# Optimization experiments

Hardware: AMD Instinct MI355X
Metric: run time of the kernel (lower is better)

## Reference

```python
import jax, jax.numpy as jnp
import numpy as np

# Model constants (from TinyRecursiveModel defaults)
IN = 200        # input feature dim (hard-coded Linear(200, d_model))
D = 64          # d_model
NH = 2          # nhead (head_dim = 32); with seq_len=1 attention is trivial
FF = 64         # dim_feedforward
LAYERS = 2      # TransformerEncoder num_layers
STEPS = 16      # recursion_steps
B = 65536       # batch size
EPS = 1e-5      # torch LayerNorm eps


def setup_inputs() -> dict:
    key = jax.random.key(0)
    ks = jax.random.split(key, 14)
    w = lambda k, shape, s=0.05: (jax.random.normal(k, shape, jnp.float32) * s)
    return {
        "x": jax.random.normal(ks[0], (B, IN), jnp.float32),
        # input_proj: Linear(200, 64)
        "input_w": w(ks[1], (D, IN)), "input_b": w(ks[2], (D,)),
        # per-layer MHA: packed in_proj (q,k,v) and out_proj, stacked over LAYERS
        "Wqkv": w(ks[3], (LAYERS, 3 * D, D)), "bqkv": w(ks[4], (LAYERS, 3 * D)),
        "Wo": w(ks[5], (LAYERS, D, D)), "bo": w(ks[6], (LAYERS, D)),
        "ln1_g": jnp.ones((LAYERS, D), jnp.float32), "ln1_b": jnp.zeros((LAYERS, D), jnp.float32),
        # per-layer FFN: Linear(64,64) -> relu -> Linear(64,64)
        "W1": w(ks[7], (LAYERS, FF, D)), "b1": w(ks[8], (LAYERS, FF)),
        "W2": w(ks[9], (LAYERS, D, FF)), "b2": w(ks[10], (LAYERS, D)),
        "ln2_g": jnp.ones((LAYERS, D), jnp.float32), "ln2_b": jnp.zeros((LAYERS, D), jnp.float32),
        # output_proj: Linear(64, 1)
        "out_w": w(ks[11], (1, D)), "out_b": w(ks[12], (1,)),
    }


def _ln(x, g, b):
    m = jnp.mean(x, axis=-1, keepdims=True)
    v = jnp.var(x, axis=-1, keepdims=True)
    return (x - m) * jax.lax.rsqrt(v + EPS) * g + b


def reference(x, input_w, input_b, Wqkv, bqkv, Wo, bo, ln1_g, ln1_b,
              W1, b1, W2, b2, ln2_g, ln2_b, out_w, out_b):
    h = x @ input_w.T + input_b  # [B, D]; seq dim of size 1 is kept implicit

    def layer(h, l):
        # seq_len == 1: softmax over a single key is identically 1, so the
        # attention output equals V exactly (Q/K have zero influence & zero grad).
        Wv = Wqkv[l, 2 * D:3 * D]
        bv = bqkv[l, 2 * D:3 * D]
        v = h @ Wv.T + bv                     # [B, D]
        sa = v @ Wo[l].T + bo[l]              # out_proj
        h = _ln(h + sa, ln1_g[l], ln1_b[l])   # post-norm (torch default)
        ff = jax.nn.relu(h @ W1[l].T + b1[l]) @ W2[l].T + b2[l]
        return _ln(h + ff, ln2_g[l], ln2_b[l])

    def step(h, _):
        for l in range(LAYERS):  # 2 structurally distinct layers
            h = layer(h, l)
        return h, None

    h, _ = jax.lax.scan(step, h, None, length=STEPS)
    out = h @ out_w.T + out_b  # [B, 1]
    return out[:, 0]           # squeeze -> [B]
```

## Files before the change

### kernel.cpp

```cpp
#include <hip/hip_runtime.h>


using f16x8 = __attribute__((ext_vector_type(8))) _Float16;
using f16x2 = __attribute__((ext_vector_type(2))) _Float16;
using f32x4 = __attribute__((ext_vector_type(4))) float;

#define DI __device__ __forceinline__

namespace {

constexpr int RS = 144;
constexpr float EPS = 1e-5f;

DI unsigned pkrtz(float a, float b) {
#if __has_builtin(__builtin_amdgcn_cvt_pkrtz)
  return __builtin_bit_cast(unsigned, __builtin_amdgcn_cvt_pkrtz(a, b));
#else
  unsigned r;
  asm("v_cvt_pkrtz_f16_f32 %0, %1, %2" : "=v"(r) : "v"(a), "v"(b));
  return r;
#endif
}

DI f16x8 cvt8h(f32x4 a, f32x4 b) {
  f16x8 r;
  r[0] = (_Float16)a[0]; r[1] = (_Float16)a[1];
  r[2] = (_Float16)a[2]; r[3] = (_Float16)a[3];
  r[4] = (_Float16)b[0]; r[5] = (_Float16)b[1];
  r[6] = (_Float16)b[2]; r[7] = (_Float16)b[3];
  return r;
}

DI unsigned pkmax0(unsigned t) {
  unsigned r;
  asm("v_pk_max_f16 %0, %1, 0" : "=v"(r) : "v"(t));
  return r;
}

DI void swap16(unsigned& a, unsigned& b) {
#if __has_builtin(__builtin_amdgcn_permlane16_swap)
  auto r = __builtin_amdgcn_permlane16_swap(a, b, false, false);
  a = r[0]; b = r[1];
#else
  unsigned ax = (unsigned)__shfl_xor((int)a, 16);
  unsigned bx = (unsigned)__shfl_xor((int)b, 16);
  bool odd = (threadIdx.x & 16) != 0;
  unsigned na = odd ? bx : a;
  unsigned nb = odd ? b : ax;
  a = na; b = nb;
#endif
}
DI void swap32(unsigned& a, unsigned& b) {
#if __has_builtin(__builtin_amdgcn_permlane32_swap)
  auto r = __builtin_amdgcn_permlane32_swap(a, b, false, false);
  a = r[0]; b = r[1];
#else
  unsigned ax = (unsigned)__shfl_xor((int)a, 32);
  unsigned bx = (unsigned)__shfl_xor((int)b, 32);
  bool hi = (threadIdx.x & 32) != 0;
  unsigned na = hi ? bx : a;
  unsigned nb = hi ? b : ax;
  a = na; b = nb;
#endif
}

DI float reduce4(float x) {
  unsigned a = __builtin_bit_cast(unsigned, x), b = a;
  swap16(a, b);
  float x1 = __builtin_bit_cast(float, a) + __builtin_bit_cast(float, b);
  unsigned c = __builtin_bit_cast(unsigned, x1), d = c;
  swap32(c, d);
  return __builtin_bit_cast(float, c) + __builtin_bit_cast(float, d);
}

union BU {
  unsigned u[8];
  struct { f16x8 b0, b1; } f;
};

template <bool RELU>
DI void packacc(const f32x4 (&acc)[4], BU& o) {
#pragma unroll
  for (int tp = 0; tp < 4; ++tp) {
    unsigned p0 = pkrtz(acc[tp][0], acc[tp][1]);
    unsigned p1 = pkrtz(acc[tp][2], acc[tp][3]);
    if (RELU) { p0 = pkmax0(p0); p1 = pkmax0(p1); }
    o.u[2 * tp + 0] = p0;
    o.u[2 * tp + 1] = p1;
  }
}

struct WFrag { f16x8 f[4][2]; };

DI WFrag loadW(const float* W, int l15, int g) {
  WFrag w;
#pragma unroll
  for (int tp = 0; tp < 4; ++tp)
#pragma unroll
    for (int s = 0; s < 2; ++s) {
      const float* p = W + (16 * tp + l15) * 64 + 32 * s + 4 * g;
      w.f[tp][s] = cvt8h(*(const f32x4*)p, *(const f32x4*)(p + 16));
    }
  return w;
}

DI f32x4 mfma(f16x8 a, f16x8 b, f32x4 c) {
  return __builtin_amdgcn_mfma_f32_16x16x32_f16(a, b, c, 0, 0, 0);
}

DI void lnorm2(const f32x4 (&aA)[4], const f32x4 (&aB)[4], const float* gb,
               int g, f32x4 (&hA)[4], f32x4 (&hB)[4]) {
  float sA = 0.f, qA = 0.f, sB = 0.f, qB = 0.f;
#pragma unroll
  for (int tp = 0; tp < 4; ++tp)
#pragma unroll
    for (int r = 0; r < 4; ++r) {
      float xa = aA[tp][r]; sA += xa; qA = fmaf(xa, xa, qA);
      float xb = aB[tp][r]; sB += xb; qB = fmaf(xb, xb, qB);
    }
  sA = reduce4(sA); qA = reduce4(qA);
  sB = reduce4(sB); qB = reduce4(qB);
  float mA = sA * 0.015625f, mB = sB * 0.015625f;
  float rA = rsqrtf(fmaf(qA, 0.015625f, -mA * mA) + EPS);
  float rB = rsqrtf(fmaf(qB, 0.015625f, -mB * mB) + EPS);
  float uA = -mA * rA, uB = -mB * rB;
  const f32x4* gv = (const f32x4*)gb;
#pragma unroll
  for (int tp = 0; tp < 4; ++tp) {
    f32x4 gg = gv[4 * tp + g];
    f32x4 bb = gv[16 + 4 * tp + g];
#pragma unroll
    for (int r = 0; r < 4; ++r) {
      hA[tp][r] = fmaf(fmaf(aA[tp][r], rA, uA), gg[r], bb[r]);
      hB[tp][r] = fmaf(fmaf(aB[tp][r], rB, uB), gg[r], bb[r]);
    }
  }
}

struct alignas(16) Smem {
  char mats[4][64 * RS];
};

DI void do_layer(f32x4 (&hA)[4], f32x4 (&hB)[4], BU& bA, BU& bB,
                 const WFrag& wvo, const char* w1b, const char* w2b,
                 const float* prm, int g) {
  asm("" : "+r"(prm));
  const f32x4* pv = (const f32x4*)prm;
  f32x4 aA[4], aB[4];
#pragma unroll
  for (int tp = 0; tp < 4; ++tp) {
    aA[tp] = mfma(wvo.f[tp][1], bA.f.b1, mfma(wvo.f[tp][0], bA.f.b0, hA[tp]));
    aB[tp] = mfma(wvo.f[tp][1], bB.f.b1, mfma(wvo.f[tp][0], bB.f.b0, hB[tp]));
    f32x4 bv = pv[4 * tp + g];
    aA[tp] += bv; aB[tp] += bv;
  }
  lnorm2(aA, aB, prm + 192, g, hA, hB);
  packacc<false>(hA, bA); packacc<false>(hB, bB);
#pragma unroll
  for (int tp = 0; tp < 4; ++tp) {
    f16x8 a0 = *(const f16x8*)(w1b + tp * 16 * RS);
    f16x8 a1 = *(const f16x8*)(w1b + tp * 16 * RS + 64);
    f32x4 cin = pv[16 + 4 * tp + g];
    aA[tp] = mfma(a1, bA.f.b1, mfma(a0, bA.f.b0, cin));
    aB[tp] = mfma(a1, bB.f.b1, mfma(a0, bB.f.b0, cin));
  }
  packacc<true>(aA, bA); packacc<true>(aB, bB);
#pragma unroll
  for (int tp = 0; tp < 4; ++tp) {
    f16x8 a0 = *(const f16x8*)(w2b + tp * 16 * RS);
    f16x8 a1 = *(const f16x8*)(w2b + tp * 16 * RS + 64);
    aA[tp] = mfma(a1, bA.f.b1, mfma(a0, bA.f.b0, hA[tp]));
    aB[tp] = mfma(a1, bB.f.b1, mfma(a0, bB.f.b0, hB[tp]));
    f32x4 bv = pv[32 + 4 * tp + g];
    aA[tp] += bv; aB[tp] += bv;
  }
  lnorm2(aA, aB, prm + 320, g, hA, hB);
  packacc<false>(hA, bA); packacc<false>(hB, bB);
}

__global__ __launch_bounds__(256) void precompute_kernel(
    const float* __restrict__ Wqkv, const float* __restrict__ bqkv,
    const float* __restrict__ Wo, const float* __restrict__ bo,
    const float* __restrict__ b1, const float* __restrict__ b2,
    const float* __restrict__ ln1_g, const float* __restrict__ ln1_b,
    const float* __restrict__ ln2_g, const float* __restrict__ ln2_b,
    float* __restrict__ ws) {
  __shared__ float wv[4096];
  __shared__ float wo[4096];
  const int l = blockIdx.x;
  const float* Wv  = Wqkv + l * (192 * 64) + 128 * 64;
  const float* WoL = Wo + l * 4096;
  for (int e = threadIdx.x; e < 4096; e += 256) { wv[e] = Wv[e]; wo[e] = WoL[e]; }
  __syncthreads();
  float* wvo = ws + l * 4096;
  const int i = threadIdx.x >> 2, j0 = (threadIdx.x & 3) * 16;
  float acc[16];
#pragma unroll
  for (int jj = 0; jj < 16; ++jj) acc[jj] = 0.f;
  for (int k = 0; k < 64; ++k) {
    float a = wo[i * 64 + k];
#pragma unroll
    for (int jj = 0; jj < 16; ++jj) acc[jj] = fmaf(a, wv[k * 64 + j0 + jj], acc[jj]);
  }
#pragma unroll
  for (int jj = 0; jj < 16; ++jj) wvo[i * 64 + j0 + jj] = acc[jj];
  float* prm = ws + 2 * 4096 + l * 448;
  if (threadIdx.x < 64) {
    const int i2 = threadIdx.x;
    const float* bv = bqkv + l * 192 + 128;
    float s = bo[l * 64 + i2];
    for (int k = 0; k < 64; ++k) s = fmaf(wo[i2 * 64 + k], bv[k], s);
    prm[i2]       = s;
    prm[64 + i2]  = b1[l * 64 + i2];
    prm[128 + i2] = b2[l * 64 + i2];
    prm[192 + i2] = ln1_g[l * 64 + i2];
    prm[256 + i2] = ln1_b[l * 64 + i2];
    prm[320 + i2] = ln2_g[l * 64 + i2];
    prm[384 + i2] = ln2_b[l * 64 + i2];
  }
}

__global__ __launch_bounds__(256, 2) void trm8_kernel(
    const float* __restrict__ x, const float* __restrict__ input_w,
    const float* __restrict__ input_b, const float* __restrict__ W1,
    const float* __restrict__ W2, const float* __restrict__ out_w,
    const float* __restrict__ out_b, const float* __restrict__ ws,
    float* __restrict__ out) {
  __shared__ Smem sm;
  const int tid = threadIdx.x;
  const int w = tid >> 6, lane = tid & 63;
  const int l15 = lane & 15, g = lane >> 4;
  const int row0 = blockIdx.x * 128 + w * 32;

  {
    const float* srcs[4] = {W1, W1 + 4096, W2, W2 + 4096};
#pragma unroll
    for (int m = 0; m < 4; ++m) {
      char* dst = sm.mats[m];
      const float* src = srcs[m];
      for (int e = tid; e < 512; e += 256) {
        int row = e >> 3, q = e & 7, s = q >> 2, gq = q & 3;
        const float* p = src + row * 64 + 32 * s + 4 * gq;
        *(f16x8*)(dst + row * RS + 64 * s + 16 * gq) =
            cvt8h(*(const f32x4*)p, *(const f32x4*)(p + 16));
      }
    }
  }

  WFrag wvo0 = loadW(ws, l15, g);
  WFrag wvo1 = loadW(ws + 4096, l15, g);

  const char* w1b0 = sm.mats[0] + l15 * RS + 16 * g;
  const char* w1b1 = sm.mats[1] + l15 * RS + 16 * g;
  const char* w2b0 = sm.mats[2] + l15 * RS + 16 * g;
  const char* w2b1 = sm.mats[3] + l15 * RS + 16 * g;
  const float* prm0 = ws + 2 * 4096;
  const float* prm1 = ws + 2 * 4096 + 448;

  f32x4 hA[4], hB[4];
#pragma unroll
  for (int tp = 0; tp < 4; ++tp) {
    f32x4 ib = *(const f32x4*)(input_b + 16 * tp + 4 * g);
    hA[tp] = ib; hB[tp] = ib;
  }
  {
    const float* xA = x + (size_t)(row0 + l15) * 200;
    const float* xB = xA + 16 * 200;
    const f32x4 zero = {0.f, 0.f, 0.f, 0.f};
    for (int s7 = 0; s7 < 7; ++s7) {
      int kb = 32 * s7 + 8 * g;
      bool v0 = kb < 200;
      f32x4 xa0 = v0 ? *(const f32x4*)(xA + kb) : zero;
      f32x4 xa1 = v0 ? *(const f32x4*)(xA + kb + 4) : zero;
      f32x4 xb0 = v0 ? *(const f32x4*)(xB + kb) : zero;
      f32x4 xb1 = v0 ? *(const f32x4*)(xB + kb + 4) : zero;
      f16x8 bfA = cvt8h(xa0, xa1);
      f16x8 bfB = cvt8h(xb0, xb1);
#pragma unroll
      for (int tp = 0; tp < 4; ++tp) {
        const float* wr = input_w + (16 * tp + l15) * 200;
        f32x4 wa = v0 ? *(const f32x4*)(wr + kb) : zero;
        f32x4 wb = v0 ? *(const f32x4*)(wr + kb + 4) : zero;
        f16x8 af = cvt8h(wa, wb);
        hA[tp] = mfma(af, bfA, hA[tp]);
        hB[tp] = mfma(af, bfB, hB[tp]);
      }
    }
  }
  BU bA, bB;
  packacc<false>(hA, bA); packacc<false>(hB, bB);
  __syncthreads();

#pragma unroll 1
  for (int step = 0; step < 16; ++step) {
    do_layer(hA, hB, bA, bB, wvo0, w1b0, w2b0, prm0, g);
    do_layer(hA, hB, bA, bB, wvo1, w1b1, w2b1, prm1, g);
  }

  float pA = 0.f, pB = 0.f;
#pragma unroll
  for (int tp = 0; tp < 4; ++tp) {
    f32x4 ow = *(const f32x4*)(out_w + 16 * tp + 4 * g);
#pragma unroll
    for (int r = 0; r < 4; ++r) {
      pA = fmaf(hA[tp][r], ow[r], pA);
      pB = fmaf(hB[tp][r], ow[r], pB);
    }
  }
  pA += __shfl_xor(pA, 16); pA += __shfl_xor(pA, 32);
  pB += __shfl_xor(pB, 16); pB += __shfl_xor(pB, 32);
  if (lane < 16) {
    float ob = out_b[0];
    out[row0 + l15]      = pA + ob;
    out[row0 + 16 + l15] = pB + ob;
  }
}

}

extern "C" void kernel_launch(void* const* d_in, const int* in_sizes, int n_in,
                              void* d_out, int out_size, void* d_ws, size_t ws_size,
                              hipStream_t stream) {
  const float* x       = (const float*)d_in[0];
  const float* input_w = (const float*)d_in[1];
  const float* input_b = (const float*)d_in[2];
  const float* Wqkv    = (const float*)d_in[3];
  const float* bqkv    = (const float*)d_in[4];
  const float* Wo      = (const float*)d_in[5];
  const float* bo      = (const float*)d_in[6];
  const float* ln1_g   = (const float*)d_in[7];
  const float* ln1_b   = (const float*)d_in[8];
  const float* W1      = (const float*)d_in[9];
  const float* b1      = (const float*)d_in[10];
  const float* W2      = (const float*)d_in[11];
  const float* b2      = (const float*)d_in[12];
  const float* ln2_g   = (const float*)d_in[13];
  const float* ln2_b   = (const float*)d_in[14];
  const float* out_w   = (const float*)d_in[15];
  const float* out_b   = (const float*)d_in[16];
  float* out = (float*)d_out;
  float* ws  = (float*)d_ws;

  hipLaunchKernelGGL(precompute_kernel, dim3(2), dim3(256), 0, stream,
                     Wqkv, bqkv, Wo, bo, b1, b2, ln1_g, ln1_b, ln2_g, ln2_b, ws);
  hipLaunchKernelGGL(trm8_kernel, dim3(512), dim3(256), 0, stream,
                     x, input_w, input_b, W1, W2, out_w, out_b, ws, out);
}
```

Measured before the change: 108.2 us.

## Process four 16-row tiles per wavefront with 128-thread blocks

```diff
diff --git a/kernel.cpp b/kernel.cpp
--- a/kernel.cpp
+++ b/kernel.cpp
@@ -2,7 +2,6 @@
 
 
 using f16x8 = __attribute__((ext_vector_type(8))) _Float16;
-using f16x2 = __attribute__((ext_vector_type(2))) _Float16;
 using f32x4 = __attribute__((ext_vector_type(4))) float;
 
 #define DI __device__ __forceinline__
@@ -108,22 +107,32 @@
   return __builtin_amdgcn_mfma_f32_16x16x32_f16(a, b, c, 0, 0, 0);
 }
 
-DI void lnorm2(const f32x4 (&aA)[4], const f32x4 (&aB)[4], const float* gb,
-               int g, f32x4 (&hA)[4], f32x4 (&hB)[4]) {
-  float sA = 0.f, qA = 0.f, sB = 0.f, qB = 0.f;
+DI void lnorm4(const f32x4 (&a0)[4], const f32x4 (&a1)[4],
+               const f32x4 (&a2)[4], const f32x4 (&a3)[4],
+               const float* gb, int g,
+               f32x4 (&h0)[4], f32x4 (&h1)[4], f32x4 (&h2)[4], f32x4 (&h3)[4]) {
+  float s0 = 0.f, q0 = 0.f, s1 = 0.f, q1 = 0.f;
+  float s2 = 0.f, q2 = 0.f, s3 = 0.f, q3 = 0.f;
 #pragma unroll
   for (int tp = 0; tp < 4; ++tp)
 #pragma unroll
     for (int r = 0; r < 4; ++r) {
-      float xa = aA[tp][r]; sA += xa; qA = fmaf(xa, xa, qA);
-      float xb = aB[tp][r]; sB += xb; qB = fmaf(xb, xb, qB);
-    }
-  sA = reduce4(sA); qA = reduce4(qA);
-  sB = reduce4(sB); qB = reduce4(qB);
-  float mA = sA * 0.015625f, mB = sB * 0.015625f;
-  float rA = rsqrtf(fmaf(qA, 0.015625f, -mA * mA) + EPS);
-  float rB = rsqrtf(fmaf(qB, 0.015625f, -mB * mB) + EPS);
-  float uA = -mA * rA, uB = -mB * rB;
+      float x0 = a0[tp][r]; s0 += x0; q0 = fmaf(x0, x0, q0);
+      float x1 = a1[tp][r]; s1 += x1; q1 = fmaf(x1, x1, q1);
+      float x2 = a2[tp][r]; s2 += x2; q2 = fmaf(x2, x2, q2);
+      float x3 = a3[tp][r]; s3 += x3; q3 = fmaf(x3, x3, q3);
+    }
+  s0 = reduce4(s0); q0 = reduce4(q0);
+  s1 = reduce4(s1); q1 = reduce4(q1);
+  s2 = reduce4(s2); q2 = reduce4(q2);
+  s3 = reduce4(s3); q3 = reduce4(q3);
+  float m0 = s0 * 0.015625f, m1 = s1 * 0.015625f;
+  float m2 = s2 * 0.015625f, m3 = s3 * 0.015625f;
+  float r0 = rsqrtf(fmaf(q0, 0.015625f, -m0 * m0) + EPS);
+  float r1 = rsqrtf(fmaf(q1, 0.015625f, -m1 * m1) + EPS);
+  float r2 = rsqrtf(fmaf(q2, 0.015625f, -m2 * m2) + EPS);
+  float r3 = rsqrtf(fmaf(q3, 0.015625f, -m3 * m3) + EPS);
+  float u0 = -m0 * r0, u1 = -m1 * r1, u2 = -m2 * r2, u3 = -m3 * r3;
   const f32x4* gv = (const f32x4*)gb;
 #pragma unroll
   for (int tp = 0; tp < 4; ++tp) {
@@ -131,8 +140,10 @@
     f32x4 bb = gv[16 + 4 * tp + g];
 #pragma unroll
     for (int r = 0; r < 4; ++r) {
-      hA[tp][r] = fmaf(fmaf(aA[tp][r], rA, uA), gg[r], bb[r]);
-      hB[tp][r] = fmaf(fmaf(aB[tp][r], rB, uB), gg[r], bb[r]);
+      h0[tp][r] = fmaf(fmaf(a0[tp][r], r0, u0), gg[r], bb[r]);
+      h1[tp][r] = fmaf(fmaf(a1[tp][r], r1, u1), gg[r], bb[r]);
+      h2[tp][r] = fmaf(fmaf(a2[tp][r], r2, u2), gg[r], bb[r]);
+      h3[tp][r] = fmaf(fmaf(a3[tp][r], r3, u3), gg[r], bb[r]);
     }
   }
 }
@@ -141,41 +152,48 @@
   char mats[4][64 * RS];
 };
 
-DI void do_layer(f32x4 (&hA)[4], f32x4 (&hB)[4], BU& bA, BU& bB,
-                 const WFrag& wvo, const char* w1b, const char* w2b,
-                 const float* prm, int g) {
+DI void do_layer(f32x4 (&h0)[4], f32x4 (&h1)[4], f32x4 (&h2)[4], f32x4 (&h3)[4],
+                 BU& b0, BU& b1, BU& b2, BU& b3, const WFrag& wvo,
+                 const char* w1b, const char* w2b, const float* prm, int g) {
   asm("" : "+r"(prm));
   const f32x4* pv = (const f32x4*)prm;
-  f32x4 aA[4], aB[4];
-#pragma unroll
-  for (int tp = 0; tp < 4; ++tp) {
-    aA[tp] = mfma(wvo.f[tp][1], bA.f.b1, mfma(wvo.f[tp][0], bA.f.b0, hA[tp]));
-    aB[tp] = mfma(wvo.f[tp][1], bB.f.b1, mfma(wvo.f[tp][0], bB.f.b0, hB[tp]));
+  f32x4 a0[4], a1[4], a2[4], a3[4];
+#pragma unroll
+  for (int tp = 0; tp < 4; ++tp) {
     f32x4 bv = pv[4 * tp + g];
-    aA[tp] += bv; aB[tp] += bv;
-  }
-  lnorm2(aA, aB, prm + 192, g, hA, hB);
-  packacc<false>(hA, bA); packacc<false>(hB, bB);
-#pragma unroll
-  for (int tp = 0; tp < 4; ++tp) {
-    f16x8 a0 = *(const f16x8*)(w1b + tp * 16 * RS);
-    f16x8 a1 = *(const f16x8*)(w1b + tp * 16 * RS + 64);
+    a0[tp] = mfma(wvo.f[tp][1], b0.f.b1, mfma(wvo.f[tp][0], b0.f.b0, h0[tp])) + bv;
+    a1[tp] = mfma(wvo.f[tp][1], b1.f.b1, mfma(wvo.f[tp][0], b1.f.b0, h1[tp])) + bv;
+    a2[tp] = mfma(wvo.f[tp][1], b2.f.b1, mfma(wvo.f[tp][0], b2.f.b0, h2[tp])) + bv;
+    a3[tp] = mfma(wvo.f[tp][1], b3.f.b1, mfma(wvo.f[tp][0], b3.f.b0, h3[tp])) + bv;
+  }
+  lnorm4(a0, a1, a2, a3, prm + 192, g, h0, h1, h2, h3);
+  packacc<false>(h0, b0); packacc<false>(h1, b1);
+  packacc<false>(h2, b2); packacc<false>(h3, b3);
+#pragma unroll
+  for (int tp = 0; tp < 4; ++tp) {
+    f16x8 wa0 = *(const f16x8*)(w1b + tp * 16 * RS);
+    f16x8 wa1 = *(const f16x8*)(w1b + tp * 16 * RS + 64);
     f32x4 cin = pv[16 + 4 * tp + g];
-    aA[tp] = mfma(a1, bA.f.b1, mfma(a0, bA.f.b0, cin));
-    aB[tp] = mfma(a1, bB.f.b1, mfma(a0, bB.f.b0, cin));
-  }
-  packacc<true>(aA, bA); packacc<true>(aB, bB);
-#pragma unroll
-  for (int tp = 0; tp < 4; ++tp) {
-    f16x8 a0 = *(const f16x8*)(w2b + tp * 16 * RS);
-    f16x8 a1 = *(const f16x8*)(w2b + tp * 16 * RS + 64);
-    aA[tp] = mfma(a1, bA.f.b1, mfma(a0, bA.f.b0, hA[tp]));
-    aB[tp] = mfma(a1, bB.f.b1, mfma(a0, bB.f.b0, hB[tp]));
+    a0[tp] = mfma(wa1, b0.f.b1, mfma(wa0, b0.f.b0, cin));
+    a1[tp] = mfma(wa1, b1.f.b1, mfma(wa0, b1.f.b0, cin));
+    a2[tp] = mfma(wa1, b2.f.b1, mfma(wa0, b2.f.b0, cin));
+    a3[tp] = mfma(wa1, b3.f.b1, mfma(wa0, b3.f.b0, cin));
+  }
+  packacc<true>(a0, b0); packacc<true>(a1, b1);
+  packacc<true>(a2, b2); packacc<true>(a3, b3);
+#pragma unroll
+  for (int tp = 0; tp < 4; ++tp) {
+    f16x8 wa0 = *(const f16x8*)(w2b + tp * 16 * RS);
+    f16x8 wa1 = *(const f16x8*)(w2b + tp * 16 * RS + 64);
     f32x4 bv = pv[32 + 4 * tp + g];
-    aA[tp] += bv; aB[tp] += bv;
-  }
-  lnorm2(aA, aB, prm + 320, g, hA, hB);
-  packacc<false>(hA, bA); packacc<false>(hB, bB);
+    a0[tp] = mfma(wa1, b0.f.b1, mfma(wa0, b0.f.b0, h0[tp])) + bv;
+    a1[tp] = mfma(wa1, b1.f.b1, mfma(wa0, b1.f.b0, h1[tp])) + bv;
+    a2[tp] = mfma(wa1, b2.f.b1, mfma(wa0, b2.f.b0, h2[tp])) + bv;
+    a3[tp] = mfma(wa1, b3.f.b1, mfma(wa0, b3.f.b0, h3[tp])) + bv;
+  }
+  lnorm4(a0, a1, a2, a3, prm + 320, g, h0, h1, h2, h3);
+  packacc<false>(h0, b0); packacc<false>(h1, b1);
+  packacc<false>(h2, b2); packacc<false>(h3, b3);
 }
 
 __global__ __launch_bounds__(256) void precompute_kernel(
@@ -220,7 +238,7 @@
   }
 }
 
-__global__ __launch_bounds__(256, 2) void trm8_kernel(
+__global__ __launch_bounds__(128, 2) void trm10_kernel(
     const float* __restrict__ x, const float* __restrict__ input_w,
     const float* __restrict__ input_b, const float* __restrict__ W1,
     const float* __restrict__ W2, const float* __restrict__ out_w,
@@ -230,7 +248,7 @@
   const int tid = threadIdx.x;
   const int w = tid >> 6, lane = tid & 63;
   const int l15 = lane & 15, g = lane >> 4;
-  const int row0 = blockIdx.x * 128 + w * 32;
+  const int row0 = blockIdx.x * 128 + w * 64;
 
   {
     const float* srcs[4] = {W1, W1 + 4096, W2, W2 + 4096};
@@ -238,7 +256,7 @@
     for (int m = 0; m < 4; ++m) {
       char* dst = sm.mats[m];
       const float* src = srcs[m];
-      for (int e = tid; e < 512; e += 256) {
+      for (int e = tid; e < 512; e += 128) {
         int row = e >> 3, q = e & 7, s = q >> 2, gq = q & 3;
         const float* p = src + row * 64 + 32 * s + 4 * gq;
         *(f16x8*)(dst + row * RS + 64 * s + 16 * gq) =
@@ -257,62 +275,75 @@
   const float* prm0 = ws + 2 * 4096;
   const float* prm1 = ws + 2 * 4096 + 448;
 
-  f32x4 hA[4], hB[4];
+  f32x4 h0[4], h1[4], h2[4], h3[4];
 #pragma unroll
   for (int tp = 0; tp < 4; ++tp) {
     f32x4 ib = *(const f32x4*)(input_b + 16 * tp + 4 * g);
-    hA[tp] = ib; hB[tp] = ib;
+    h0[tp] = ib; h1[tp] = ib; h2[tp] = ib; h3[tp] = ib;
   }
   {
-    const float* xA = x + (size_t)(row0 + l15) * 200;
-    const float* xB = xA + 16 * 200;
+    const float* xr0 = x + (size_t)(row0 + l15) * 200;
+    const float* xr1 = xr0 + 16 * 200;
+    const float* xr2 = xr0 + 32 * 200;
+    const float* xr3 = xr0 + 48 * 200;
     const f32x4 zero = {0.f, 0.f, 0.f, 0.f};
     for (int s7 = 0; s7 < 7; ++s7) {
       int kb = 32 * s7 + 8 * g;
       bool v0 = kb < 200;
-      f32x4 xa0 = v0 ? *(const f32x4*)(xA + kb) : zero;
-      f32x4 xa1 = v0 ? *(const f32x4*)(xA + kb + 4) : zero;
-      f32x4 xb0 = v0 ? *(const f32x4*)(xB + kb) : zero;
-      f32x4 xb1 = v0 ? *(const f32x4*)(xB + kb + 4) : zero;
-      f16x8 bfA = cvt8h(xa0, xa1);
-      f16x8 bfB = cvt8h(xb0, xb1);
+      f16x8 bf0 = cvt8h(v0 ? *(const f32x4*)(xr0 + kb) : zero,
+                        v0 ? *(const f32x4*)(xr0 + kb + 4) : zero);
+      f16x8 bf1 = cvt8h(v0 ? *(const f32x4*)(xr1 + kb) : zero,
+                        v0 ? *(const f32x4*)(xr1 + kb + 4) : zero);
+      f16x8 bf2 = cvt8h(v0 ? *(const f32x4*)(xr2 + kb) : zero,
+                        v0 ? *(const f32x4*)(xr2 + kb + 4) : zero);
+      f16x8 bf3 = cvt8h(v0 ? *(const f32x4*)(xr3 + kb) : zero,
+                        v0 ? *(const f32x4*)(xr3 + kb + 4) : zero);
 #pragma unroll
       for (int tp = 0; tp < 4; ++tp) {
         const float* wr = input_w + (16 * tp + l15) * 200;
         f32x4 wa = v0 ? *(const f32x4*)(wr + kb) : zero;
         f32x4 wb = v0 ? *(const f32x4*)(wr + kb + 4) : zero;
         f16x8 af = cvt8h(wa, wb);
-        hA[tp] = mfma(af, bfA, hA[tp]);
-        hB[tp] = mfma(af, bfB, hB[tp]);
+        h0[tp] = mfma(af, bf0, h0[tp]);
+        h1[tp] = mfma(af, bf1, h1[tp]);
+        h2[tp] = mfma(af, bf2, h2[tp]);
+        h3[tp] = mfma(af, bf3, h3[tp]);
       }
     }
   }
-  BU bA, bB;
-  packacc<false>(hA, bA); packacc<false>(hB, bB);
+  BU b0, b1, b2, b3;
+  packacc<false>(h0, b0); packacc<false>(h1, b1);
+  packacc<false>(h2, b2); packacc<false>(h3, b3);
   __syncthreads();
 
 #pragma unroll 1
   for (int step = 0; step < 16; ++step) {
-    do_layer(hA, hB, bA, bB, wvo0, w1b0, w2b0, prm0, g);
-    do_layer(hA, hB, bA, bB, wvo1, w1b1, w2b1, prm1, g);
-  }
-
-  float pA = 0.f, pB = 0.f;
+    do_layer(h0, h1, h2, h3, b0, b1, b2, b3, wvo0, w1b0, w2b0, prm0, g);
+    do_layer(h0, h1, h2, h3, b0, b1, b2, b3, wvo1, w1b1, w2b1, prm1, g);
+  }
+
+  float p0 = 0.f, p1 = 0.f, p2 = 0.f, p3 = 0.f;
 #pragma unroll
   for (int tp = 0; tp < 4; ++tp) {
     f32x4 ow = *(const f32x4*)(out_w + 16 * tp + 4 * g);
 #pragma unroll
     for (int r = 0; r < 4; ++r) {
-      pA = fmaf(hA[tp][r], ow[r], pA);
-      pB = fmaf(hB[tp][r], ow[r], pB);
-    }
-  }
-  pA += __shfl_xor(pA, 16); pA += __shfl_xor(pA, 32);
-  pB += __shfl_xor(pB, 16); pB += __shfl_xor(pB, 32);
+      p0 = fmaf(h0[tp][r], ow[r], p0);
+      p1 = fmaf(h1[tp][r], ow[r], p1);
+      p2 = fmaf(h2[tp][r], ow[r], p2);
+      p3 = fmaf(h3[tp][r], ow[r], p3);
+    }
+  }
+  p0 += __shfl_xor(p0, 16); p0 += __shfl_xor(p0, 32);
+  p1 += __shfl_xor(p1, 16); p1 += __shfl_xor(p1, 32);
+  p2 += __shfl_xor(p2, 16); p2 += __shfl_xor(p2, 32);
+  p3 += __shfl_xor(p3, 16); p3 += __shfl_xor(p3, 32);
   if (lane < 16) {
     float ob = out_b[0];
-    out[row0 + l15]      = pA + ob;
-    out[row0 + 16 + l15] = pB + ob;
+    out[row0 + l15]      = p0 + ob;
+    out[row0 + 16 + l15] = p1 + ob;
+    out[row0 + 32 + l15] = p2 + ob;
+    out[row0 + 48 + l15] = p3 + ob;
   }
 }
 
@@ -343,6 +374,6 @@
 
   hipLaunchKernelGGL(precompute_kernel, dim3(2), dim3(256), 0, stream,
                      Wqkv, bqkv, Wo, bo, b1, b2, ln1_g, ln1_b, ln2_g, ln2_b, ws);
-  hipLaunchKernelGGL(trm8_kernel, dim3(512), dim3(256), 0, stream,
+  hipLaunchKernelGGL(trm10_kernel, dim3(512), dim3(128), 0, stream,
                      x, input_w, input_b, W1, W2, out_w, out_b, ws, out);
 }
```

Result: slower. 166.5 us (+53.9%).
